# Kernel tuning notes

Hardware: AMD Instinct MI355X
Metric: run time of the kernel (lower is better)

The kernel has to match this reference:

```python
import jax, jax.numpy as jnp
import numpy as np
from jax import lax

D_MODEL = 1024
D_STATE = 16
D_CONV = 4
D_INNER = 2048  # expand * d_model
DT_RANK = 64    # ceil(d_model / 16)
BATCH = 2
SEQ = 2048


def setup_inputs() -> dict:
    key = jax.random.key(0)
    ks = jax.random.split(key, 8)
    s = 0.02
    x = jax.random.normal(ks[0], (BATCH, SEQ, D_MODEL), jnp.float32)
    in_proj_w = jax.random.normal(ks[1], (2 * D_INNER, D_MODEL), jnp.float32) * s
    conv_w = jax.random.normal(ks[2], (D_INNER, 1, D_CONV), jnp.float32) * s  # [out, in/groups, k]
    conv_b = jax.random.normal(ks[3], (D_INNER,), jnp.float32) * s
    x_proj_w = jax.random.normal(ks[4], (DT_RANK + 2 * D_STATE, D_INNER), jnp.float32) * s
    dt_proj_w = jax.random.normal(ks[5], (D_INNER, DT_RANK), jnp.float32) * s
    dt_proj_b = jax.random.normal(ks[6], (D_INNER,), jnp.float32) * s
    A_log = jnp.log(jnp.tile(jnp.arange(1, D_STATE + 1, dtype=jnp.float32), (D_INNER, 1)))
    D = jnp.ones((D_INNER,), jnp.float32)
    out_proj_w = jax.random.normal(ks[7], (D_MODEL, D_INNER), jnp.float32) * s
    return dict(x=x, in_proj_w=in_proj_w, conv_w=conv_w, conv_b=conv_b,
                x_proj_w=x_proj_w, dt_proj_w=dt_proj_w, dt_proj_b=dt_proj_b,
                A_log=A_log, D=D, out_proj_w=out_proj_w)


def _causal_depthwise_conv(x_bcl, conv_w, conv_b):
    # x_bcl: [B, d_inner, L]; conv_w: [d_inner, 1, k]; left-pad k-1 -> causal, output length L
    y = lax.conv_general_dilated(
        x_bcl, conv_w,
        window_strides=(1,), padding=[(D_CONV - 1, 0)],
        feature_group_count=D_INNER,
        dimension_numbers=('NCH', 'OIH', 'NCH'))
    return y + conv_b[None, :, None]


def _ssm(xc, x_proj_w, dt_proj_w, dt_proj_b, A_log, D):
    # xc: [B, L, d_inner]
    A = -jnp.exp(A_log)                                   # [d, N]
    x_dbl = jnp.einsum('bld,rd->blr', xc, x_proj_w)       # [B, L, dt_rank + 2N]
    dt_low = x_dbl[..., :DT_RANK]
    Bm = x_dbl[..., DT_RANK:DT_RANK + D_STATE]            # [B, L, N]
    Cm = x_dbl[..., DT_RANK + D_STATE:]                   # [B, L, N]
    dt = jax.nn.softplus(jnp.einsum('blr,dr->bld', dt_low, dt_proj_w) + dt_proj_b)  # [B, L, d]
    dA = jnp.exp(dt[..., None] * A)                       # [B, L, d, N]
    dBx = dt[..., None] * Bm[:, :, None, :] * xc[..., None]  # [B, L, d, N]

    def step(h, inp):
        dA_t, dBx_t, C_t = inp                            # [B,d,N], [B,d,N], [B,N]
        h = dA_t * h + dBx_t
        y = jnp.einsum('bdn,bn->bd', h, C_t)
        return h, y

    h0 = jnp.zeros((xc.shape[0], D_INNER, D_STATE), xc.dtype)
    _, ys = lax.scan(step, h0,
                     (dA.transpose(1, 0, 2, 3), dBx.transpose(1, 0, 2, 3), Cm.transpose(1, 0, 2)))
    y = ys.transpose(1, 0, 2)                             # [B, L, d]
    return y + xc * D


def reference(x, in_proj_w, conv_w, conv_b, x_proj_w, dt_proj_w, dt_proj_b, A_log, D, out_proj_w):
    xz = jnp.einsum('blm,om->blo', x, in_proj_w)          # [B, L, 2*d_inner]
    xs, z = jnp.split(xz, 2, axis=-1)
    xc = _causal_depthwise_conv(xs.transpose(0, 2, 1), conv_w, conv_b).transpose(0, 2, 1)
    xc = jax.nn.silu(xc)
    y = _ssm(xc, x_proj_w, dt_proj_w, dt_proj_b, A_log, D)
    out = y * jax.nn.silu(z)
    return jnp.einsum('bld,md->blm', out, out_proj_w)
```

## Files before the change

kernel.cpp:

```cpp
#include <hip/hip_runtime.h>

#define SEQ    2048
#define DIN    2048
#define DMODEL 1024
#define NROWS  4096
#define NCH    64
#define CHL    32

typedef __attribute__((ext_vector_type(8))) _Float16 half8v;
typedef __attribute__((ext_vector_type(8))) unsigned short ushort8v;
typedef __attribute__((ext_vector_type(4))) float f32x4;

__device__ __forceinline__ float sigf(float x) { return 1.0f / (1.0f + __expf(-x)); }
__device__ __forceinline__ float softplusf(float v) {
    return fmaxf(v, 0.f) + __logf(1.f + __expf(-fabsf(v)));
}

__device__ __forceinline__ void gload16(const void* g, const void* l) {
    __builtin_amdgcn_global_load_lds((const __attribute__((address_space(1))) void*)g,
                                     (__attribute__((address_space(3))) void*)l, 16, 0, 0);
}

__device__ __forceinline__ unsigned short f2h(float x) {
    _Float16 h = (_Float16)x;
    unsigned short u;
    __builtin_memcpy(&u, &h, 2);
    return u;
}
__device__ __forceinline__ float h2f(unsigned short u) {
    _Float16 h;
    __builtin_memcpy(&h, &u, 2);
    return (float)h;
}

__global__ __launch_bounds__(256) void cvt_in_k(
    const float* __restrict__ x, const float* __restrict__ wi, const float* __restrict__ wx,
    const float* __restrict__ wd, const float* __restrict__ wo,
    unsigned short* __restrict__ xh, unsigned short* __restrict__ wih,
    unsigned short* __restrict__ wxh, unsigned short* __restrict__ wdh,
    unsigned short* __restrict__ woh)
{
    int i = blockIdx.x * 256 + threadIdx.x;
    if (i < 1048576) {
        float4 v = ((const float4*)x)[i];
        ushort4 h; h.x = f2h(v.x); h.y = f2h(v.y); h.z = f2h(v.z); h.w = f2h(v.w);
        ((ushort4*)xh)[i] = h;
    } else if (i < 2097152) {
        i -= 1048576;
        float4 v = ((const float4*)wi)[i];
        ushort4 h; h.x = f2h(v.x); h.y = f2h(v.y); h.z = f2h(v.z); h.w = f2h(v.w);
        ((ushort4*)wih)[i] = h;
    } else if (i < 2162688) {
        i -= 2097152;
        int row = i >> 9, q = i & 511;
        ushort4 h;
        if (row < 96) {
            float4 v = ((const float4*)wx)[(size_t)row * 512 + q];
            h.x = f2h(v.x); h.y = f2h(v.y); h.z = f2h(v.z); h.w = f2h(v.w);
        } else h = make_ushort4(0, 0, 0, 0);
        ((ushort4*)wxh)[(size_t)row * 512 + q] = h;
    } else if (i < 2195456) {
        i -= 2162688;
        float4 v = ((const float4*)wd)[i];
        ushort4 h; h.x = f2h(v.x); h.y = f2h(v.y); h.z = f2h(v.z); h.w = f2h(v.w);
        ((ushort4*)wdh)[i] = h;
    } else {
        i -= 2195456;
        float4 v = ((const float4*)wo)[i];
        ushort4 h; h.x = f2h(v.x); h.y = f2h(v.y); h.z = f2h(v.z); h.w = f2h(v.w);
        ((ushort4*)woh)[i] = h;
    }
}

__global__ __launch_bounds__(512, 4) void gemm_inproj(
    const unsigned short* __restrict__ A, const unsigned short* __restrict__ W,
    unsigned short* __restrict__ C, int K, int N, int mtiles, int lda, int ldw)
{
    __shared__ uint4 ldsu4[3072];
    char* lds = (char*)ldsu4;
    const int tid = threadIdx.x;
    const int w = tid >> 6, lane = tid & 63;

    const int nwg = gridDim.x;
    const int cpx = nwg >> 3;
    const int bid = blockIdx.x;
    const int swz = (bid & 7) * cpx + (bid >> 3);
    const int ntiles = nwg / mtiles;
    const int per = 8 * ntiles;
    const int gid = swz / per;
    const int rem = swz - gid * per;
    const int m0 = (gid * 8 + (rem & 7)) * 256;
    const int n0 = (rem >> 3) * 128;

    const int wr = w >> 2, wc = w & 3;
    const int lm = lane & 15, lk = lane >> 4;

    f32x4 acc[8][2];
#pragma unroll
    for (int i = 0; i < 8; ++i)
#pragma unroll
        for (int j = 0; j < 2; ++j) { acc[i][j][0]=0.f; acc[i][j][1]=0.f; acc[i][j][2]=0.f; acc[i][j][3]=0.f; }

    const int rsub = w * 8 + (lane >> 3);
    const int xr8  = ((lane & 7) ^ (lane >> 3)) << 3;
    const unsigned short* gA = A + (size_t)(m0 + rsub) * lda + xr8;
    const unsigned short* gW = W + (size_t)(n0 + rsub) * ldw + xr8;
    const int sdst = w * 1024;

    for (int kt = 0; kt < K; kt += 64) {
#pragma unroll
        for (int i = 0; i < 4; ++i)
            gload16(gA + (size_t)i * 64 * lda + kt, lds + i * 8192 + sdst);
#pragma unroll
        for (int i = 0; i < 2; ++i)
            gload16(gW + (size_t)i * 64 * ldw + kt, lds + 32768 + i * 8192 + sdst);
        __syncthreads();
#pragma unroll
        for (int kk = 0; kk < 2; ++kk) {
            half8v b[2];
#pragma unroll
            for (int nb = 0; nb < 2; ++nb) {
                const int br = wc * 32 + nb * 16 + lm;
                b[nb] = *(const half8v*)(lds + 32768 + br * 128 + (((kk * 4 + lk) ^ (br & 7)) << 4));
            }
            __builtin_amdgcn_s_setprio(1);
#pragma unroll
            for (int mb = 0; mb < 8; ++mb) {
                const int ar = wr * 128 + mb * 16 + lm;
                half8v a = *(const half8v*)(lds + ar * 128 + (((kk * 4 + lk) ^ (ar & 7)) << 4));
#pragma unroll
                for (int nb = 0; nb < 2; ++nb)
                    acc[mb][nb] = __builtin_amdgcn_mfma_f32_16x16x32_f16(a, b[nb], acc[mb][nb], 0, 0, 0);
            }
            __builtin_amdgcn_s_setprio(0);
        }
        __syncthreads();
    }

#pragma unroll
    for (int mb = 0; mb < 8; ++mb)
#pragma unroll
        for (int nb = 0; nb < 2; ++nb)
#pragma unroll
            for (int r = 0; r < 4; ++r)
                C[(size_t)(m0 + wr * 128 + mb * 16 + lk * 4 + r) * N + (n0 + wc * 32 + nb * 16 + lm)]
                    = f2h(acc[mb][nb][r]);
}

#define A_OFF 0
#define W_OFF 16384

__global__ __launch_bounds__(256) void gemm_mfma_h(
    const unsigned short* __restrict__ A, const unsigned short* __restrict__ W,
    unsigned short* __restrict__ C, int K, int ldc, int nmax, int mtiles,
    int sA1, int sA2, int ldw, const float* __restrict__ bias, int kspl, int cstride)
{
    __shared__ uint4 ldsu4[2048];
    char* lds = (char*)ldsu4;
    const int tid  = threadIdx.x;
    const int w    = tid >> 6, lane = tid & 63;

    const int nwg = gridDim.x;
    const int cpx = nwg >> 3;
    const int bid = blockIdx.x;
    const int swz = (bid & 7) * cpx + (bid >> 3);
    const int nbp = nwg / kspl;
    const int ks  = swz / nbp;
    const int tt  = swz - ks * nbp;
    const int ntiles = nbp / mtiles;
    const int per = 8 * ntiles;
    const int gid = tt / per;
    const int rem = tt - gid * per;
    const int m0 = (gid * 8 + (rem & 7)) * 128;
    const int n0 = (rem >> 3) * 128;
    const int kOff = ks * K;

    const int wr = w >> 1, wc = w & 1;

    f32x4 acc[4][4];
#pragma unroll
    for (int i = 0; i < 4; ++i)
#pragma unroll
        for (int j = 0; j < 4; ++j) { acc[i][j][0]=0.f; acc[i][j][1]=0.f; acc[i][j][2]=0.f; acc[i][j][3]=0.f; }

    const int rloc = w * 32 + (lane >> 3);
    const int xr8  = ((lane & 7) ^ (lane >> 3)) << 3;
    const int rowA = m0 + rloc;
    const unsigned short* gA = A + (size_t)(rowA >> 1) * sA2 + (size_t)(rowA & 1) * sA1 + kOff + xr8;
    const unsigned short* gW = W + (size_t)(n0 + rloc) * ldw + kOff + xr8;

    const int lm  = lane & 15;
    const int lk  = lane >> 4;
    const int lk4 = lk * 4;

    for (int kt = 0; kt < K; kt += 64) {
#pragma unroll
        for (int i = 0; i < 4; ++i) {
            const int rb = w * 32 + i * 8;
            gload16(gA + (size_t)i * 4 * sA2 + kt, lds + A_OFF + rb * 128);
            gload16(gW + (size_t)i * 8 * ldw + kt, lds + W_OFF + rb * 128);
        }
        __syncthreads();
#pragma unroll
        for (int h = 0; h < 2; ++h) {
            half8v af[4], wf[4];
            const int ch = h * 4 + lk;
#pragma unroll
            for (int t = 0; t < 4; ++t) {
                const int ar = wr * 64 + t * 16 + lm;
                const int wrw = wc * 64 + t * 16 + lm;
                af[t] = *(const half8v*)(lds + A_OFF + ar * 128 + ((ch ^ (ar & 7)) << 4));
                wf[t] = *(const half8v*)(lds + W_OFF + wrw * 128 + ((ch ^ (wrw & 7)) << 4));
            }
#pragma unroll
            for (int i = 0; i < 4; ++i)
#pragma unroll
                for (int j = 0; j < 4; ++j)
                    acc[i][j] = __builtin_amdgcn_mfma_f32_16x16x32_f16(af[i], wf[j], acc[i][j], 0, 0, 0);
        }
        __syncthreads();
    }

    unsigned short* Cp = C + (size_t)ks * cstride;
    if (bias) {
#pragma unroll
        for (int j = 0; j < 4; ++j) {
            const int n = n0 + wc * 64 + j * 16 + lm;
            const float bv = (n < nmax) ? bias[n] : 0.f;
#pragma unroll
            for (int i = 0; i < 4; ++i)
#pragma unroll
                for (int r = 0; r < 4; ++r) {
                    float v = acc[i][j][r] + bv;
                    if (n < nmax)
                        Cp[(size_t)(m0 + wr * 64 + i * 16 + lk4 + r) * ldc + n] = f2h(softplusf(v));
                }
        }
    } else {
#pragma unroll
        for (int i = 0; i < 4; ++i)
#pragma unroll
            for (int j = 0; j < 4; ++j) {
                const int n = n0 + wc * 64 + j * 16 + lm;
                if (n < nmax)
#pragma unroll
                    for (int r = 0; r < 4; ++r)
                        Cp[(size_t)(m0 + wr * 64 + i * 16 + lk4 + r) * ldc + n] = f2h(acc[i][j][r]);
            }
    }
}

__global__ __launch_bounds__(256) void xproj_reduce_k(
    const unsigned short* __restrict__ part, float* __restrict__ xdbl,
    unsigned short* __restrict__ dlh)
{
    int i = blockIdx.x * 256 + threadIdx.x;
    if (i >= NROWS * 32) return;
    int row = i >> 5, q = i & 31;
    float s0 = 0.f, s1 = 0.f, s2 = 0.f, s3 = 0.f;
#pragma unroll
    for (int ks = 0; ks < 8; ++ks) {
        ushort4 v = *(const ushort4*)(part + (size_t)ks * (NROWS * 128) + (size_t)row * 128 + q * 4);
        s0 += h2f(v.x); s1 += h2f(v.y); s2 += h2f(v.z); s3 += h2f(v.w);
    }
    if (q < 16) {
        ushort4 h; h.x = f2h(s0); h.y = f2h(s1); h.z = f2h(s2); h.w = f2h(s3);
        *(ushort4*)(dlh + (size_t)row * 64 + q * 4) = h;
    } else {
        *(float4*)(xdbl + (size_t)row * 96 + q * 4) = make_float4(s0, s1, s2, s3);
    }
}

__global__ __launch_bounds__(256) void out_reduce_k(
    const unsigned short* __restrict__ p, float* __restrict__ out)
{
    int i = blockIdx.x * 256 + threadIdx.x;
    ushort4 a = ((const ushort4*)p)[i];
    ushort4 b = ((const ushort4*)(p + 4194304))[i];
    float4 v;
    v.x = h2f(a.x) + h2f(b.x);
    v.y = h2f(a.y) + h2f(b.y);
    v.z = h2f(a.z) + h2f(b.z);
    v.w = h2f(a.w) + h2f(b.w);
    ((float4*)out)[i] = v;
}

__global__ __launch_bounds__(256) void conv_silu_k(
    const unsigned short* __restrict__ xzh, const float* __restrict__ cw,
    const float* __restrict__ cb, unsigned short* __restrict__ xch)
{
    int i = blockIdx.x * 256 + threadIdx.x;
    int d8 = (i & 255) << 3;
    int row = i >> 8;
    int l = row & (SEQ - 1);
    const unsigned short* base = xzh + (size_t)row * 4096 + d8;
    ushort8v x0 = *(const ushort8v*)base;
    ushort8v x1 = {}, x2 = {}, x3 = {};
    if (l >= 1) x1 = *(const ushort8v*)(base - 4096);
    if (l >= 2) x2 = *(const ushort8v*)(base - 8192);
    if (l >= 3) x3 = *(const ushort8v*)(base - 12288);
    ushort8v out;
#pragma unroll
    for (int j = 0; j < 8; ++j) {
        float4 wv = *(const float4*)(cw + (size_t)(d8 + j) * 4);
        float a = cb[d8 + j];
        a = fmaf(h2f(x3[j]), wv.x, a);
        a = fmaf(h2f(x2[j]), wv.y, a);
        a = fmaf(h2f(x1[j]), wv.z, a);
        a = fmaf(h2f(x0[j]), wv.w, a);
        out[j] = f2h(a * sigf(a));
    }
    *(ushort8v*)(xch + (size_t)row * DIN + d8) = out;
}

__global__ __launch_bounds__(256) void scan_pass1(
    const unsigned short* __restrict__ dth, const unsigned short* __restrict__ xch,
    const float* __restrict__ xdbl, const float* __restrict__ Alog,
    unsigned short* __restrict__ hbuf, unsigned short* __restrict__ apbuf)
{
    const int b = blockIdx.z, c = blockIdx.y;
    const int d = blockIdx.x * 256 + threadIdx.x;
    float A[16];
#pragma unroll
    for (int q = 0; q < 4; ++q) *(float4*)&A[q * 4] = *(const float4*)&Alog[(size_t)d * 16 + q * 4];
    bool seq = true;
#pragma unroll
    for (int n = 0; n < 16; ++n) {
        A[n] = -__expf(A[n]);
        seq = seq && (fabsf(A[n] + (float)(n + 1)) < 1e-5f * (float)(n + 1));
    }
    float h[16] = {};
    float sumdt = 0.f;
    const int rowbase = b * SEQ + c * CHL;
    int row = rowbase;
    float dtv = h2f(dth[(size_t)row * DIN + d]);
    float xcv = h2f(xch[(size_t)row * DIN + d]);
    if (seq) {
        for (int t = 0; t < CHL; ++t) {
            const int nrow = row + ((t + 1) < CHL ? 1 : 0);
            float dtv2 = h2f(dth[(size_t)nrow * DIN + d]);
            float xcv2 = h2f(xch[(size_t)nrow * DIN + d]);
            const float* xr = xdbl + (size_t)row * 96;
            float u = dtv * xcv;
            sumdt += dtv;
            float r = __expf(-dtv);
            float dA = r;
#pragma unroll
            for (int n = 0; n < 16; ++n) {
                h[n] = fmaf(dA, h[n], u * xr[64 + n]);
                dA *= r;
            }
            dtv = dtv2; xcv = xcv2; row = nrow;
        }
    } else {
        for (int t = 0; t < CHL; ++t) {
            const int nrow = row + ((t + 1) < CHL ? 1 : 0);
            float dtv2 = h2f(dth[(size_t)nrow * DIN + d]);
            float xcv2 = h2f(xch[(size_t)nrow * DIN + d]);
            const float* xr = xdbl + (size_t)row * 96;
            float u = dtv * xcv;
            sumdt += dtv;
#pragma unroll
            for (int n = 0; n < 16; ++n) {
                float dA = __expf(dtv * A[n]);
                h[n] = fmaf(dA, h[n], u * xr[64 + n]);
            }
            dtv = dtv2; xcv = xcv2; row = nrow;
        }
    }
    float ap[16];
    if (seq) {
        float R = __expf(-sumdt);
        float a = R;
#pragma unroll
        for (int n = 0; n < 16; ++n) { ap[n] = a; a *= R; }
    } else {
#pragma unroll
        for (int n = 0; n < 16; ++n) ap[n] = __expf(sumdt * A[n]);
    }
    size_t e = ((size_t)(b * NCH + c) << 15) + (size_t)d * 16;
    ushort8v hv0, hv1, av0, av1;
#pragma unroll
    for (int n = 0; n < 8; ++n) {
        hv0[n] = f2h(h[n]);  hv1[n] = f2h(h[8 + n]);
        av0[n] = f2h(ap[n]); av1[n] = f2h(ap[8 + n]);
    }
    *(ushort8v*)(hbuf + e)      = hv0;
    *(ushort8v*)(hbuf + e + 8)  = hv1;
    *(ushort8v*)(apbuf + e)     = av0;
    *(ushort8v*)(apbuf + e + 8) = av1;
}

__global__ __launch_bounds__(256) void scan_pass2(
    unsigned short* __restrict__ hbuf, const unsigned short* __restrict__ apbuf)
{
    int idx = blockIdx.x * 256 + threadIdx.x;
    int b = idx >> 15;
    int dn = idx & 32767;
    float carry = 0.f;
    for (int c = 0; c < NCH; ++c) {
        size_t e = ((size_t)(b * NCH + c) << 15) + dn;
        float hl = h2f(hbuf[e]);
        float ap = h2f(apbuf[e]);
        hbuf[e] = f2h(carry);
        carry = fmaf(ap, carry, hl);
    }
}

__global__ __launch_bounds__(256) void scan_pass3(
    const unsigned short* __restrict__ dth, const unsigned short* __restrict__ xch,
    const unsigned short* __restrict__ xzh, const float* __restrict__ xdbl,
    const float* __restrict__ Alog, const float* __restrict__ Dp,
    const unsigned short* __restrict__ hbuf, unsigned short* __restrict__ oph)
{
    const int b = blockIdx.z, c = blockIdx.y;
    const int d = blockIdx.x * 256 + threadIdx.x;
    float A[16];
#pragma unroll
    for (int q = 0; q < 4; ++q) *(float4*)&A[q * 4] = *(const float4*)&Alog[(size_t)d * 16 + q * 4];
    bool seq = true;
#pragma unroll
    for (int n = 0; n < 16; ++n) {
        A[n] = -__expf(A[n]);
        seq = seq && (fabsf(A[n] + (float)(n + 1)) < 1e-5f * (float)(n + 1));
    }
    float h[16];
    size_t e = ((size_t)(b * NCH + c) << 15) + (size_t)d * 16;
    {
        ushort8v hv0 = *(const ushort8v*)(hbuf + e);
        ushort8v hv1 = *(const ushort8v*)(hbuf + e + 8);
#pragma unroll
        for (int n = 0; n < 8; ++n) { h[n] = h2f(hv0[n]); h[8 + n] = h2f(hv1[n]); }
    }
    const float Dd = Dp[d];
    const int rowbase = b * SEQ + c * CHL;
    int row = rowbase;
    float dtv = h2f(dth[(size_t)row * DIN + d]);
    float xcv = h2f(xch[(size_t)row * DIN + d]);
    float zv  = h2f(xzh[(size_t)row * 4096 + DIN + d]);
    if (seq) {
        for (int t = 0; t < CHL; ++t) {
            const int nrow = row + ((t + 1) < CHL ? 1 : 0);
            float dtv2 = h2f(dth[(size_t)nrow * DIN + d]);
            float xcv2 = h2f(xch[(size_t)nrow * DIN + d]);
            float zv2  = h2f(xzh[(size_t)nrow * 4096 + DIN + d]);
            const float* xr = xdbl + (size_t)row * 96;
            float u = dtv * xcv;
            float r = __expf(-dtv);
            float dA = r;
            float y = 0.f;
#pragma unroll
            for (int n = 0; n < 16; ++n) {
                h[n] = fmaf(dA, h[n], u * xr[64 + n]);
                y = fmaf(h[n], xr[80 + n], y);
                dA *= r;
            }
            float val = (y + xcv * Dd) * zv * sigf(zv);
            oph[(size_t)row * DIN + d] = f2h(val);
            dtv = dtv2; xcv = xcv2; zv = zv2; row = nrow;
        }
    } else {
        for (int t = 0; t < CHL; ++t) {
            const int nrow = row + ((t + 1) < CHL ? 1 : 0);
            float dtv2 = h2f(dth[(size_t)nrow * DIN + d]);
            float xcv2 = h2f(xch[(size_t)nrow * DIN + d]);
            float zv2  = h2f(xzh[(size_t)nrow * 4096 + DIN + d]);
            const float* xr = xdbl + (size_t)row * 96;
            float u = dtv * xcv;
            float y = 0.f;
#pragma unroll
            for (int n = 0; n < 16; ++n) {
                float dA = __expf(dtv * A[n]);
                h[n] = fmaf(dA, h[n], u * xr[64 + n]);
                y = fmaf(h[n], xr[80 + n], y);
            }
            float val = (y + xcv * Dd) * zv * sigf(zv);
            oph[(size_t)row * DIN + d] = f2h(val);
            dtv = dtv2; xcv = xcv2; zv = zv2; row = nrow;
        }
    }
}

extern "C" void kernel_launch(void* const* d_in, const int* in_sizes, int n_in,
                              void* d_out, int out_size, void* d_ws, size_t ws_size,
                              hipStream_t stream)
{
    const float* x    = (const float*)d_in[0];
    const float* wi   = (const float*)d_in[1];
    const float* cw   = (const float*)d_in[2];
    const float* cb   = (const float*)d_in[3];
    const float* wx   = (const float*)d_in[4];
    const float* wd   = (const float*)d_in[5];
    const float* bd   = (const float*)d_in[6];
    const float* alog = (const float*)d_in[7];
    const float* Dp   = (const float*)d_in[8];
    const float* wo   = (const float*)d_in[9];
    float* out = (float*)d_out;

    float* wsf  = (float*)d_ws;
    float* xzr  = wsf;
    float* xcr  = wsf + 16777216;
    float* xdbl = wsf + 25165824;
    float* dtr  = wsf + 25559040;

    unsigned short* xzh = (unsigned short*)xzr;
    float* scr = xzr + 8388608;
    unsigned short* oph  = (unsigned short*)scr;
    unsigned short* hbuf = (unsigned short*)(scr + 4194304);

    unsigned short* xh    = (unsigned short*)xcr;
    unsigned short* xch   = (unsigned short*)xcr;
    unsigned short* apbuf = (unsigned short*)(xcr + 4194304);

    unsigned short* wih    = (unsigned short*)dtr;
    unsigned short* dth    = (unsigned short*)dtr;
    unsigned short* oparth = (unsigned short*)dtr;
    unsigned short* wxh    = (unsigned short*)(dtr + 4194304);
    unsigned short* xparth = (unsigned short*)(dtr + 4325376);
    unsigned short* woh    = (unsigned short*)(dtr + 6422528);
    unsigned short* wdh    = (unsigned short*)(dtr + 7471104);
    unsigned short* dlh    = (unsigned short*)(dtr + 7536640);

    cvt_in_k<<<10624, 256, 0, stream>>>(x, wi, wx, wd, wo, xh, wih, wxh, wdh, woh);
    gemm_inproj<<<512, 512, 0, stream>>>(xh, wih, xzh, 1024, 4096, 16, 1024, 1024);
    conv_silu_k<<<4096, 256, 0, stream>>>(xzh, cw, cb, xch);
    gemm_mfma_h<<<256, 256, 0, stream>>>(xch, wxh, xparth, 256, 128, 128, 32, 2048, 4096, 2048,
                                         nullptr, 8, NROWS * 128);
    xproj_reduce_k<<<512, 256, 0, stream>>>(xparth, xdbl, dlh);
    gemm_mfma_h<<<512, 256, 0, stream>>>(dlh, wdh, dth, 64, 2048, 2048, 32, 64, 128, 64,
                                         bd, 1, 0);
    scan_pass1<<<dim3(8, NCH, 2), 256, 0, stream>>>(dth, xch, xdbl, alog, hbuf, apbuf);
    scan_pass2<<<256, 256, 0, stream>>>(hbuf, apbuf);
    scan_pass3<<<dim3(8, NCH, 2), 256, 0, stream>>>(dth, xch, xzh, xdbl, alog, Dp, hbuf, oph);
    gemm_mfma_h<<<512, 256, 0, stream>>>(oph, woh, oparth, 1024, 1024, 1024, 32, 2048, 4096, 2048,
                                         nullptr, 2, 4194304);
    out_reduce_k<<<4096, 256, 0, stream>>>(oparth, out);
}
```

Baseline: 183.5 us.

## Replace split-K out-projection GEMM and reduce with direct fp32 GEMM

```diff
diff --git a/kernel.cpp b/kernel.cpp
--- a/kernel.cpp
+++ b/kernel.cpp
@@ -147,6 +147,81 @@
                     = f2h(acc[mb][nb][r]);
 }
 
+__global__ __launch_bounds__(256, 4) void gemm_out(
+    const unsigned short* __restrict__ A, const unsigned short* __restrict__ W,
+    float* __restrict__ C, int K, int N, int mtiles, int lda, int ldw)
+{
+    __shared__ uint4 ldsu4[1536];
+    char* lds = (char*)ldsu4;
+    const int tid = threadIdx.x;
+    const int w = tid >> 6, lane = tid & 63;
+
+    const int nwg = gridDim.x;
+    const int cpx = nwg >> 3;
+    const int bid = blockIdx.x;
+    const int swz = (bid & 7) * cpx + (bid >> 3);
+    const int ntiles = nwg / mtiles;
+    const int per = 8 * ntiles;
+    const int gid = swz / per;
+    const int rem = swz - gid * per;
+    const int m0 = (gid * 8 + (rem & 7)) * 128;
+    const int n0 = (rem >> 3) * 64;
+
+    const int wr = w >> 1, wc = w & 1;
+    const int lm = lane & 15, lk = lane >> 4;
+
+    f32x4 acc[4][2];
+#pragma unroll
+    for (int i = 0; i < 4; ++i)
+#pragma unroll
+        for (int j = 0; j < 2; ++j) { acc[i][j][0]=0.f; acc[i][j][1]=0.f; acc[i][j][2]=0.f; acc[i][j][3]=0.f; }
+
+    const int rloc = w * 8 + (lane >> 3);
+    const int xr8  = ((lane & 7) ^ (lane >> 3)) << 3;
+    const unsigned short* gA = A + (size_t)(m0 + rloc) * lda + xr8;
+    const unsigned short* gW = W + (size_t)(n0 + rloc) * ldw + xr8;
+    const int sdst = w * 1024;
+
+    for (int kt = 0; kt < K; kt += 64) {
+#pragma unroll
+        for (int i = 0; i < 4; ++i)
+            gload16(gA + (size_t)i * 32 * lda + kt, lds + i * 4096 + sdst);
+#pragma unroll
+        for (int i = 0; i < 2; ++i)
+            gload16(gW + (size_t)i * 32 * ldw + kt, lds + 16384 + i * 4096 + sdst);
+        __syncthreads();
+#pragma unroll
+        for (int kk = 0; kk < 2; ++kk) {
+            half8v b[2];
+#pragma unroll
+            for (int nb = 0; nb < 2; ++nb) {
+                const int br = wc * 32 + nb * 16 + lm;
+                b[nb] = *(const half8v*)(lds + 16384 + br * 128 + (((kk * 4 + lk) ^ (br & 7)) << 4));
+            }
+            __builtin_amdgcn_s_setprio(1);
+#pragma unroll
+            for (int mb = 0; mb < 4; ++mb) {
+                const int ar = wr * 64 + mb * 16 + lm;
+                half8v a = *(const half8v*)(lds + ar * 128 + (((kk * 4 + lk) ^ (ar & 7)) << 4));
+#pragma unroll
+                for (int nb = 0; nb < 2; ++nb)
+                    acc[mb][nb] = __builtin_amdgcn_mfma_f32_16x16x32_f16(a, b[nb], acc[mb][nb], 0, 0, 0);
+            }
+            __builtin_amdgcn_s_setprio(0);
+        }
+        __syncthreads();
+    }
+
+#pragma unroll
+    for (int mb = 0; mb < 4; ++mb)
+#pragma unroll
+        for (int nb = 0; nb < 2; ++nb)
+#pragma unroll
+            for (int r = 0; r < 4; ++r)
+                C[(size_t)(m0 + wr * 64 + mb * 16 + lk * 4 + r) * N + (n0 + wc * 32 + nb * 16 + lm)]
+                    = acc[mb][nb][r];
+}
+
 #define A_OFF 0
 #define W_OFF 16384
 
@@ -269,20 +344,6 @@
     } else {
         *(float4*)(xdbl + (size_t)row * 96 + q * 4) = make_float4(s0, s1, s2, s3);
     }
-}
-
-__global__ __launch_bounds__(256) void out_reduce_k(
-    const unsigned short* __restrict__ p, float* __restrict__ out)
-{
-    int i = blockIdx.x * 256 + threadIdx.x;
-    ushort4 a = ((const ushort4*)p)[i];
-    ushort4 b = ((const ushort4*)(p + 4194304))[i];
-    float4 v;
-    v.x = h2f(a.x) + h2f(b.x);
-    v.y = h2f(a.y) + h2f(b.y);
-    v.z = h2f(a.z) + h2f(b.z);
-    v.w = h2f(a.w) + h2f(b.w);
-    ((float4*)out)[i] = v;
 }
 
 __global__ __launch_bounds__(256) void conv_silu_k(
@@ -514,7 +575,6 @@
 
     unsigned short* wih    = (unsigned short*)dtr;
     unsigned short* dth    = (unsigned short*)dtr;
-    unsigned short* oparth = (unsigned short*)dtr;
     unsigned short* wxh    = (unsigned short*)(dtr + 4194304);
     unsigned short* xparth = (unsigned short*)(dtr + 4325376);
     unsigned short* woh    = (unsigned short*)(dtr + 6422528);
@@ -532,7 +592,5 @@
     scan_pass1<<<dim3(8, NCH, 2), 256, 0, stream>>>(dth, xch, xdbl, alog, hbuf, apbuf);
     scan_pass2<<<256, 256, 0, stream>>>(hbuf, apbuf);
     scan_pass3<<<dim3(8, NCH, 2), 256, 0, stream>>>(dth, xch, xzh, xdbl, alog, Dp, hbuf, oph);
-    gemm_mfma_h<<<512, 256, 0, stream>>>(oph, woh, oparth, 1024, 1024, 1024, 32, 2048, 4096, 2048,
-                                         nullptr, 2, 4194304);
-    out_reduce_k<<<4096, 256, 0, stream>>>(oparth, out);
-}
+    gemm_out<<<512, 256, 0, stream>>>(oph, woh, out, 2048, 1024, 32, 2048, 2048);
+}
```

Result: no change. 182.0 us (-0.8%).
